# Kernel optimization log

Measured on AMD Instinct MI355X. Metric: run time of the kernel, lower is better.

The kernel has to match this reference:

```python
import jax, jax.numpy as jnp
import numpy as np

N = 131072   # number of points
C = 128      # channels
H = 8        # heads
D = C // H   # head dim = 16
K = 48       # patch (window) size
P = 3000     # number of path segments


def _build_indices():
    """Faithful numpy replica of PathAttention.get_padding_and_inverse (index-only, no_grad)."""
    rng = np.random.default_rng(0)
    lengths = rng.integers(K + 1, 3 * K, size=P)          # all > K -> padded to multiple of K
    M = int(lengths.sum())
    bpad = ((lengths + K - 1) // K) * K
    off = np.concatenate([[0], np.cumsum(lengths)])
    offp = np.concatenate([[0], np.cumsum(bpad)])
    Mpad = int(offp[-1])
    pad = np.arange(Mpad)
    unpad = np.arange(M)
    for i in range(P):
        o0, o1, p0, p1 = off[i], off[i + 1], offp[i], offp[i + 1]
        unpad[o0:o1] += p0 - o0
        b = int(lengths[i])
        if b != bpad[i]:
            r = b % K
            # replicate previous window's tail into the padded region
            pad[p1 - K + r:p1] = pad[p1 - 2 * K + r:p1 - K]
        pad[p0:p1] -= p0 - o0
    # every point appears at least once so the scatter-mean covers all N rows
    inv = np.concatenate([rng.permutation(N), rng.integers(0, N, M - N)])
    rng.shuffle(inv)
    return pad, unpad, inv


def setup_inputs() -> dict:
    pad, unpad, inv = _build_indices()
    M = unpad.shape[0]
    key = jax.random.key(0)
    ks = jax.random.split(key, 8)
    s = 0.02
    theta = jax.random.uniform(ks[1], (M, D), minval=0.0, maxval=2.0 * np.pi)
    return {
        "feat": jax.random.normal(ks[0], (N, C), jnp.float32),
        "cos": jnp.cos(theta).astype(jnp.float32),
        "sin": jnp.sin(theta).astype(jnp.float32),
        "g1": jnp.ones((C,), jnp.float32),
        "b1": jnp.zeros((C,), jnp.float32),
        "qkv_w": (jax.random.normal(ks[2], (3 * C, C)) * s).astype(jnp.float32),
        "qkv_b": jnp.zeros((3 * C,), jnp.float32),
        "proj_w": (jax.random.normal(ks[3], (C, C)) * s).astype(jnp.float32),
        "proj_b": jnp.zeros((C,), jnp.float32),
        "g2": jnp.ones((C,), jnp.float32),
        "b2": jnp.zeros((C,), jnp.float32),
        "fc1_w": (jax.random.normal(ks[4], (4 * C, C)) * s).astype(jnp.float32),
        "fc1_b": jnp.zeros((4 * C,), jnp.float32),
        "fc2_w": (jax.random.normal(ks[5], (C, 4 * C)) * s).astype(jnp.float32),
        "fc2_b": jnp.zeros((C,), jnp.float32),
        "path_inverse": jnp.asarray(inv, jnp.int32),
        "pad": jnp.asarray(pad, jnp.int32),
        "unpad": jnp.asarray(unpad, jnp.int32),
        "num_heads": H,
        "patch_size": K,
    }


def _ln(x, g, b):
    m = x.mean(-1, keepdims=True)
    v = x.var(-1, keepdims=True)
    return (x - m) / jnp.sqrt(v + 1e-5) * g + b


def reference(feat, cos, sin, g1, b1, qkv_w, qkv_b, proj_w, proj_b, g2, b2,
              fc1_w, fc1_b, fc2_w, fc2_b, path_inverse, pad, unpad,
              num_heads, patch_size):
    Np, Cc = feat.shape
    Hh = num_heads
    Dd = Cc // Hh
    Kk = patch_size
    # pre-norm + qkv projection, then path gather and pad gather
    h = _ln(feat, g1, b1)
    qkv = (h @ qkv_w.T + qkv_b)[path_inverse][pad]          # [Mpad, 3C]
    Mpad = qkv.shape[0]
    qkv = qkv.reshape(Mpad, 3, Hh, Dd)
    q, k, v = qkv[:, 0], qkv[:, 1], qkv[:, 2]               # [Mpad, H, D]
    # non-interleaved rope (flash-attn apply_rotary_emb with cos of dim D//2)
    cp = cos[pad][:, :Dd // 2][:, None, :]                  # [Mpad, 1, D/2]
    sp = sin[pad][:, :Dd // 2][:, None, :]
    def rope(x):
        x1, x2 = x[..., :Dd // 2], x[..., Dd // 2:]
        return jnp.concatenate([x1 * cp - x2 * sp, x2 * cp + x1 * sp], axis=-1)
    q = rope(q)
    k = rope(k)
    # windowed attention: all windows are exactly K after padding
    Wn = Mpad // Kk
    qw = q.reshape(Wn, Kk, Hh, Dd)
    kw = k.reshape(Wn, Kk, Hh, Dd)
    vw = v.reshape(Wn, Kk, Hh, Dd)
    scores = jnp.einsum('wqhd,wkhd->whqk', qw, kw) * (Dd ** -0.5)
    p = jax.nn.softmax(scores, axis=-1)
    o = jnp.einsum('whqk,wkhd->wqhd', p, vw).reshape(Mpad, Cc)
    # unpad gather, output projection, scatter-mean combine over overlapping paths
    o = o[unpad] @ proj_w.T + proj_b                        # [M, C]
    sums = jax.ops.segment_sum(o, path_inverse, num_segments=Np)
    cnt = jax.ops.segment_sum(jnp.ones((o.shape[0],), o.dtype), path_inverse, num_segments=Np)
    a = sums / jnp.maximum(cnt, 1.0)[:, None]
    x = feat + a
    # MLP branch
    h2 = _ln(x, g2, b2)
    m = jax.nn.gelu(h2 @ fc1_w.T + fc1_b, approximate=False) @ fc2_w.T + fc2_b
    return x + m
```

## Files before the change

### kernel.cpp

```cpp
#include <hip/hip_runtime.h>


typedef __attribute__((ext_vector_type(4))) float f32x4;
typedef __attribute__((ext_vector_type(8))) short bf16x8;
typedef __attribute__((ext_vector_type(4))) short bf16x4;

#define MFMA(a, b, c) __builtin_amdgcn_mfma_f32_16x16x32_bf16(a, b, c, 0, 0, 0)

static __device__ __forceinline__ short f2bf(float x) {
  union { float f; unsigned u; } v; v.f = x;
  unsigned r = v.u + 0x7FFFu + ((v.u >> 16) & 1u);
  return (short)(r >> 16);
}
static __device__ __forceinline__ float bf2f(short b) {
  union { unsigned u; float f; } v;
  v.u = ((unsigned)(unsigned short)b) << 16;
  return v.f;
}

__global__ void k_cvt(const float* __restrict__ s, short* __restrict__ d, int n) {
  int i = blockIdx.x * 256 + threadIdx.x;
  if (i < n) d[i] = f2bf(s[i]);
}

__global__ void k_cnt(const int* __restrict__ pinv, int* __restrict__ cnt, int M) {
  int i = blockIdx.x * 256 + threadIdx.x;
  if (i < M) atomicAdd(&cnt[pinv[i]], 1);
}

__global__ __launch_bounds__(256) void k_scan1(const int* __restrict__ cnt,
                                               int* __restrict__ lpre,
                                               int* __restrict__ bsum) {
  const int i = blockIdx.x * 256 + threadIdx.x;
  const int t = threadIdx.x, lane = t & 63, wid = t >> 6;
  int v = cnt[i];
  int x = v;
#pragma unroll
  for (int d = 1; d < 64; d <<= 1) {
    int y = __shfl_up(x, d);
    if (lane >= d) x += y;
  }
  __shared__ int wsum[4];
  if (lane == 63) wsum[wid] = x;
  __syncthreads();
  int add = 0;
#pragma unroll
  for (int wv = 0; wv < 4; wv++) add += (wv < wid) ? wsum[wv] : 0;
  lpre[i] = x + add - v;
  if (t == 255) bsum[blockIdx.x] = x + add;
}

__global__ __launch_bounds__(512) void k_scan2(int* __restrict__ bsum, int nb) {
  const int t = threadIdx.x, lane = t & 63, wid = t >> 6;
  int v = (t < nb) ? bsum[t] : 0;
  int x = v;
#pragma unroll
  for (int d = 1; d < 64; d <<= 1) {
    int y = __shfl_up(x, d);
    if (lane >= d) x += y;
  }
  __shared__ int wsum[8];
  if (lane == 63) wsum[wid] = x;
  __syncthreads();
  int add = 0;
#pragma unroll
  for (int wv = 0; wv < 8; wv++) add += (wv < wid) ? wsum[wv] : 0;
  if (t < nb) bsum[t] = x + add - v;
}

__global__ void k_place(const int* __restrict__ pinv, const int* __restrict__ lpre,
                        const int* __restrict__ bsum, int* __restrict__ cursor,
                        int* __restrict__ idxl, int M) {
  int m = blockIdx.x * 256 + threadIdx.x;
  if (m < M) {
    int n = pinv[m];
    int slot = atomicAdd(&cursor[n], 1);
    idxl[lpre[n] + bsum[n >> 8] + slot] = m;
  }
}

__global__ __launch_bounds__(256) void k1_ln_qkv(
    const float* __restrict__ feat, const float* __restrict__ g1,
    const float* __restrict__ b1, const short* __restrict__ wq,
    const float* __restrict__ bq, short* __restrict__ qkvb) {
  __shared__ short h_lds[32 * 128];
  __shared__ short o_st[32 * 384];
  const int blk = blockIdx.x, t = threadIdx.x;
  {
    const int r = t >> 3, oct = t & 7;
    const float* fp = feat + (size_t)(blk * 32 + r) * 128 + oct * 16;
    float vals[16];
    float s = 0.f, s2 = 0.f;
#pragma unroll
    for (int i = 0; i < 4; i++) {
      f32x4 v = *(const f32x4*)(fp + i * 4);
#pragma unroll
      for (int j = 0; j < 4; j++) { float x = v[j]; vals[i * 4 + j] = x; s += x; s2 += x * x; }
    }
    s += __shfl_xor(s, 1);  s += __shfl_xor(s, 2);  s += __shfl_xor(s, 4);
    s2 += __shfl_xor(s2, 1); s2 += __shfl_xor(s2, 2); s2 += __shfl_xor(s2, 4);
    float mean = s * (1.f / 128.f);
    float rstd = rsqrtf(s2 * (1.f / 128.f) - mean * mean + 1e-5f);
    const int sw = (r & 7) << 4;
#pragma unroll
    for (int gi = 0; gi < 2; gi++) {
      bf16x8 wv;
#pragma unroll
      for (int j = 0; j < 8; j++) {
        int c = oct * 16 + gi * 8 + j;
        wv[j] = f2bf((vals[gi * 8 + j] - mean) * rstd * g1[c] + b1[c]);
      }
      *(bf16x8*)((char*)h_lds + r * 256 + ((oct * 32 + gi * 16) ^ sw)) = wv;
    }
  }
  __syncthreads();
  const int wave = t >> 6, lane = t & 63, u = lane & 15, g = lane >> 4;
  f32x4 acc[2][6];
  f32x4 zz = {0.f, 0.f, 0.f, 0.f};
#pragma unroll
  for (int a = 0; a < 2; a++)
#pragma unroll
    for (int b = 0; b < 6; b++) acc[a][b] = zz;
#pragma unroll
  for (int kk = 0; kk < 4; kk++) {
    bf16x8 af[2];
#pragma unroll
    for (int rt = 0; rt < 2; rt++)
      af[rt] = *(const bf16x8*)((char*)h_lds + (rt * 16 + u) * 256 +
                                ((kk * 64 + g * 16) ^ ((u & 7) << 4)));
    bf16x8 bfr[6];
#pragma unroll
    for (int ct = 0; ct < 6; ct++) {
      int col = wave * 96 + ct * 16 + u;
      bfr[ct] = *(const bf16x8*)(wq + (size_t)col * 128 + kk * 32 + g * 8);
    }
#pragma unroll
    for (int rt = 0; rt < 2; rt++)
#pragma unroll
      for (int ct = 0; ct < 6; ct++) acc[rt][ct] = MFMA(af[rt], bfr[ct], acc[rt][ct]);
  }
#pragma unroll
  for (int rt = 0; rt < 2; rt++)
#pragma unroll
    for (int ct = 0; ct < 6; ct++) {
      int col = wave * 96 + ct * 16 + u;
      float bias = bq[col];
#pragma unroll
      for (int reg = 0; reg < 4; reg++) {
        int rowl = rt * 16 + 4 * g + reg;
        *(short*)((char*)o_st + rowl * 768 + ((col * 2) ^ (g << 5))) =
            f2bf(acc[rt][ct][reg] + bias);
      }
    }
  __syncthreads();
  for (int idx = t; idx < 1536; idx += 256) {
    int r = idx / 48, c8 = idx % 48;
    bf16x8 v = *(const bf16x8*)((char*)o_st + r * 768 +
                                ((c8 * 16) ^ ((((r >> 2) & 3)) << 5)));
    *(bf16x8*)(qkvb + ((size_t)blk * 32 + r) * 384 + c8 * 8) = v;
  }
}

__global__ __launch_bounds__(512) void k2_attn(
    const short* __restrict__ qkv, const float* __restrict__ cosb,
    const float* __restrict__ sinb, const int* __restrict__ pinv,
    const int* __restrict__ padv, const int* __restrict__ unpadv,
    short* __restrict__ ocmp) {
  __shared__ short qo_lds[48 * 136];
  __shared__ short k_lds[48 * 128];
  __shared__ short vT[8 * 16 * 64];
  __shared__ int midx_s[48];
  __shared__ int gidx_s[48];
  __shared__ int canon_s[48];
  __shared__ float cs_s[48 * 8];
  __shared__ float sn_s[48 * 8];

  const int w = blockIdx.x;
  const int t = threadIdx.x;

  if (t < 48) {
    int pp = w * 48 + t;
    int m = padv[pp];
    midx_s[t] = m;
    gidx_s[t] = pinv[m];
    canon_s[t] = (unpadv[m] == pp) ? 1 : 0;
    const float* cp = cosb + (size_t)m * 16;
    const float* sp = sinb + (size_t)m * 16;
#pragma unroll
    for (int i = 0; i < 2; i++) {
      *(f32x4*)(cs_s + t * 8 + i * 4) = *(const f32x4*)(cp + i * 4);
      *(f32x4*)(sn_s + t * 8 + i * 4) = *(const f32x4*)(sp + i * 4);
    }
  }
  __syncthreads();

  {
    const int r = t >> 3, seg = t & 7;
    if (r < 48) {
      const short* rowp = qkv + (size_t)gidx_s[r] * 384;
#pragma unroll
      for (int ci = 0; ci < 3; ci++) {
        const int c0 = seg * 48 + ci * 16;
        const int sec = c0 >> 7;
        const int hh = (c0 & 127) >> 4;
        bf16x8 lo = *(const bf16x8*)(rowp + c0);
        bf16x8 hi = *(const bf16x8*)(rowp + c0 + 8);
        if (sec < 2) {
          bf16x8 w0, w1;
#pragma unroll
          for (int j = 0; j < 8; j++) {
            float x1 = bf2f(lo[j]), x2 = bf2f(hi[j]);
            float cp = cs_s[r * 8 + j], sp2 = sn_s[r * 8 + j];
            w0[j] = f2bf(x1 * cp - x2 * sp2);
            w1[j] = f2bf(x2 * cp + x1 * sp2);
          }
          char* dst = (char*)(sec == 0 ? qo_lds : k_lds);
          int sw = (r & 7) << 4;
          *(bf16x8*)(dst + r * 256 + ((hh * 32) ^ sw)) = w0;
          *(bf16x8*)(dst + r * 256 + ((hh * 32 + 16) ^ sw)) = w1;
        } else {
#pragma unroll
          for (int d = 0; d < 16; d++) {
            short val = (d < 8) ? lo[d] : hi[d - 8];
            *(short*)((char*)vT + hh * 2048 + d * 128 + ((r * 2) ^ ((d & 7) << 3))) = val;
          }
        }
      }
    } else {
#pragma unroll
      for (int ci = 0; ci < 3; ci++) {
        const int c0 = seg * 48 + ci * 16;
        if (c0 >= 256) {
          const int hh = (c0 & 127) >> 4;
#pragma unroll
          for (int d = 0; d < 16; d++)
            *(short*)((char*)vT + hh * 2048 + d * 128 + ((r * 2) ^ ((d & 7) << 3))) = 0;
        }
      }
    }
  }
  __syncthreads();

  const int h = t >> 6, lane = t & 63, u = lane & 15, g = lane >> 4;
  const int sbase = h * 32 + g * 16;
  bf16x8 zf = {0, 0, 0, 0, 0, 0, 0, 0};
  bf16x8 kf[3], qf[3];
#pragma unroll
  for (int i = 0; i < 3; i++) {
    int kj = i * 16 + u;
    if (g < 2) {
      kf[i] = *(const bf16x8*)((char*)k_lds + kj * 256 + (sbase ^ ((kj & 7) << 4)));
      qf[i] = *(const bf16x8*)((char*)qo_lds + kj * 256 + (sbase ^ ((kj & 7) << 4)));
    } else { kf[i] = zf; qf[i] = zf; }
  }
  union UU { bf16x8 v8; bf16x4 v4[2]; };
  UU a1, a2;
  {
    const int dbase = h * 2048 + u * 128;
    const int sw = (u & 7) << 3;
    a1.v4[0] = *(const bf16x4*)((char*)vT + dbase + ((8 * g) ^ sw));
    a1.v4[1] = *(const bf16x4*)((char*)vT + dbase + ((32 + 8 * g) ^ sw));
    a2.v4[0] = *(const bf16x4*)((char*)vT + dbase + ((64 + 8 * g) ^ sw));
    a2.v4[1] = *(const bf16x4*)((char*)vT + dbase + ((96 + 8 * g) ^ sw));
  }
  __syncthreads();

  f32x4 d1[3][3];
#pragma unroll
  for (int a = 0; a < 3; a++)
#pragma unroll
    for (int b = 0; b < 3; b++) {
      f32x4 z = {0.f, 0.f, 0.f, 0.f};
      d1[a][b] = MFMA(kf[a], qf[b], z);
    }

  float rl[3];
#pragma unroll
  for (int qt = 0; qt < 3; qt++) {
    float mx = -3.0e38f;
#pragma unroll
    for (int kt = 0; kt < 3; kt++)
#pragma unroll
      for (int rr = 0; rr < 4; rr++) {
        float sv = d1[kt][qt][rr] * 0.25f;
        d1[kt][qt][rr] = sv;
        mx = fmaxf(mx, sv);
      }
    mx = fmaxf(mx, __shfl_xor(mx, 16));
    mx = fmaxf(mx, __shfl_xor(mx, 32));
    float sm = 0.f;
#pragma unroll
    for (int kt = 0; kt < 3; kt++)
#pragma unroll
      for (int rr = 0; rr < 4; rr++) {
        float e = __expf(d1[kt][qt][rr] - mx);
        d1[kt][qt][rr] = e;
        sm += e;
      }
    sm += __shfl_xor(sm, 16);
    sm += __shfl_xor(sm, 32);
    rl[qt] = 1.0f / sm;
  }

#pragma unroll
  for (int qt = 0; qt < 3; qt++) {
    UU bu1, bu2;
#pragma unroll
    for (int i = 0; i < 4; i++) {
      bu1.v8[i] = f2bf(d1[0][qt][i]);
      bu1.v8[i + 4] = f2bf(d1[1][qt][i]);
      bu2.v8[i] = f2bf(d1[2][qt][i]);
      bu2.v8[i + 4] = 0;
    }
    f32x4 z = {0.f, 0.f, 0.f, 0.f};
    f32x4 acc = MFMA(a1.v8, bu1.v8, z);
    acc = MFMA(a2.v8, bu2.v8, acc);
#pragma unroll
    for (int reg = 0; reg < 4; reg++)
      *(short*)((char*)qo_lds + (qt * 16 + u) * 272 + h * 32 + g * 8 + reg * 2) =
          f2bf(acc[reg] * rl[qt]);
  }
  __syncthreads();
  for (int idx = t; idx < 768; idx += 512) {
    int r = idx >> 4, c8 = idx & 15;
    if (canon_s[r]) {
      *(bf16x8*)(ocmp + (size_t)midx_s[r] * 128 + c8 * 8) =
          *(const bf16x8*)((char*)qo_lds + r * 272 + c8 * 16);
    }
  }
}

__global__ __launch_bounds__(256) void k3_proj(
    const short* __restrict__ ocmp, const short* __restrict__ wp,
    const float* __restrict__ pb, short* __restrict__ oproj, int M) {
  __shared__ short o_st[64 * 128];
  const int blk = blockIdx.x, t = threadIdx.x;
  const int m0 = blk * 64;
  const int wave = t >> 6, lane = t & 63, u = lane & 15, g = lane >> 4;
  f32x4 acc[4][2];
  f32x4 zz = {0.f, 0.f, 0.f, 0.f};
#pragma unroll
  for (int a = 0; a < 4; a++) { acc[a][0] = zz; acc[a][1] = zz; }
  bf16x8 zf = {0, 0, 0, 0, 0, 0, 0, 0};
#pragma unroll
  for (int kk = 0; kk < 4; kk++) {
    bf16x8 af[4];
#pragma unroll
    for (int rt = 0; rt < 4; rt++) {
      int m = m0 + rt * 16 + u;
      af[rt] = (m < M) ? *(const bf16x8*)(ocmp + (size_t)m * 128 + kk * 32 + g * 8) : zf;
    }
    bf16x8 bfr[2];
#pragma unroll
    for (int ct = 0; ct < 2; ct++) {
      int col = wave * 32 + ct * 16 + u;
      bfr[ct] = *(const bf16x8*)(wp + (size_t)col * 128 + kk * 32 + g * 8);
    }
#pragma unroll
    for (int rt = 0; rt < 4; rt++)
#pragma unroll
      for (int ct = 0; ct < 2; ct++) acc[rt][ct] = MFMA(af[rt], bfr[ct], acc[rt][ct]);
  }
#pragma unroll
  for (int rt = 0; rt < 4; rt++)
#pragma unroll
    for (int ct = 0; ct < 2; ct++) {
      int col = wave * 32 + ct * 16 + u;
      float bias = pb[col];
#pragma unroll
      for (int reg = 0; reg < 4; reg++) {
        int rowl = rt * 16 + 4 * g + reg;
        *(short*)((char*)o_st + rowl * 256 + ((col * 2) ^ (g << 5))) =
            f2bf(acc[rt][ct][reg] + bias);
      }
    }
  __syncthreads();
#pragma unroll
  for (int it = 0; it < 4; it++) {
    int idx = t + it * 256;
    int r = idx >> 4, c8 = idx & 15;
    if (m0 + r < M) {
      bf16x8 v = *(const bf16x8*)((char*)o_st + r * 256 +
                                  ((c8 * 16) ^ (((r >> 2) & 3) << 5)));
      *(bf16x8*)(oproj + (size_t)(m0 + r) * 128 + c8 * 8) = v;
    }
  }
}

__global__ __launch_bounds__(256) void k4_fused(
    const float* __restrict__ feat, float* __restrict__ dout,
    const int* __restrict__ cnt, const int* __restrict__ lpre,
    const int* __restrict__ bsum, const int* __restrict__ idxl,
    const short* __restrict__ oproj,
    const float* __restrict__ g2, const float* __restrict__ b2,
    const short* __restrict__ w1, const float* __restrict__ bb1,
    const short* __restrict__ w2, const float* __restrict__ bb2) {
  __shared__ short m_lds[32 * 512];
  const int blk = blockIdx.x, t = threadIdx.x;
  const int wave = t >> 6, lane = t & 63, u = lane & 15, g = lane >> 4;

  {
    const int r = t >> 3, oct = t & 7;
    const int n = blk * 32 + r;
    const int c = cnt[n];
    const int start = lpre[n] + bsum[n >> 8];
    float sum[16];
#pragma unroll
    for (int i = 0; i < 16; i++) sum[i] = 0.f;
    for (int j = 0; j < c; j++) {
      int m = idxl[start + j];
      const short* op = oproj + (size_t)m * 128 + oct * 16;
      bf16x8 v0 = *(const bf16x8*)op;
      bf16x8 v1 = *(const bf16x8*)(op + 8);
#pragma unroll
      for (int q = 0; q < 8; q++) { sum[q] += bf2f(v0[q]); sum[8 + q] += bf2f(v1[q]); }
    }
    const float rc = 1.0f / fmaxf((float)c, 1.0f);
    const float* fp = feat + (size_t)n * 128 + oct * 16;
    float* xp = dout + (size_t)n * 128 + oct * 16;
    float vals[16];
    float s = 0.f, s2 = 0.f;
#pragma unroll
    for (int i = 0; i < 4; i++) {
      f32x4 fv = *(const f32x4*)(fp + i * 4);
      f32x4 xv;
#pragma unroll
      for (int j = 0; j < 4; j++) {
        float x = fv[j] + sum[i * 4 + j] * rc;
        xv[j] = x; vals[i * 4 + j] = x; s += x; s2 += x * x;
      }
      *(f32x4*)(xp + i * 4) = xv;
    }
    s += __shfl_xor(s, 1);  s += __shfl_xor(s, 2);  s += __shfl_xor(s, 4);
    s2 += __shfl_xor(s2, 1); s2 += __shfl_xor(s2, 2); s2 += __shfl_xor(s2, 4);
    float mean = s * (1.f / 128.f);
    float rstd = rsqrtf(s2 * (1.f / 128.f) - mean * mean + 1e-5f);
    const int sw = (r & 7) << 4;
#pragma unroll
    for (int gi = 0; gi < 2; gi++) {
      bf16x8 wv;
#pragma unroll
      for (int j = 0; j < 8; j++) {
        int cc = oct * 16 + gi * 8 + j;
        wv[j] = f2bf((vals[gi * 8 + j] - mean) * rstd * g2[cc] + b2[cc]);
      }
      *(bf16x8*)((char*)m_lds + r * 256 + ((oct * 32 + gi * 16) ^ sw)) = wv;
    }
  }
  __syncthreads();

  f32x4 acc[2][8];
  f32x4 zz = {0.f, 0.f, 0.f, 0.f};
#pragma unroll
  for (int a = 0; a < 2; a++)
#pragma unroll
    for (int b = 0; b < 8; b++) acc[a][b] = zz;
#pragma unroll
  for (int kk = 0; kk < 4; kk++) {
    bf16x8 af[2];
#pragma unroll
    for (int rt = 0; rt < 2; rt++)
      af[rt] = *(const bf16x8*)((char*)m_lds + (rt * 16 + u) * 256 +
                                ((kk * 64 + g * 16) ^ ((u & 7) << 4)));
    bf16x8 bfr[8];
#pragma unroll
    for (int ct = 0; ct < 8; ct++) {
      int col = wave * 128 + ct * 16 + u;
      bfr[ct] = *(const bf16x8*)(w1 + (size_t)col * 128 + kk * 32 + g * 8);
    }
#pragma unroll
    for (int rt = 0; rt < 2; rt++)
#pragma unroll
      for (int ct = 0; ct < 8; ct++) acc[rt][ct] = MFMA(af[rt], bfr[ct], acc[rt][ct]);
  }
  __syncthreads();

#pragma unroll
  for (int rt = 0; rt < 2; rt++)
#pragma unroll
    for (int ct = 0; ct < 8; ct++) {
      int col = wave * 128 + ct * 16 + u;
      float bias = bb1[col];
#pragma unroll
      for (int reg = 0; reg < 4; reg++) {
        int rowl = rt * 16 + 4 * g + reg;
        float v = acc[rt][ct][reg] + bias;
        v = 0.5f * v * (1.0f + erff(v * 0.70710678118654752f));
        *(short*)((char*)m_lds + rowl * 1024 + ((col * 2) ^ ((rowl & 7) << 4))) = f2bf(v);
      }
    }
  __syncthreads();

  f32x4 acc2[2][2];
#pragma unroll
  for (int a = 0; a < 2; a++) { acc2[a][0] = zz; acc2[a][1] = zz; }
#pragma unroll
  for (int kk = 0; kk < 16; kk++) {
    bf16x8 af2[2];
#pragma unroll
    for (int rt = 0; rt < 2; rt++)
      af2[rt] = *(const bf16x8*)((char*)m_lds + (rt * 16 + u) * 1024 +
                                 ((kk * 64 + g * 16) ^ ((u & 7) << 4)));
#pragma unroll
    for (int ct = 0; ct < 2; ct++) {
      int col = wave * 32 + ct * 16 + u;
      bf16x8 bfr = *(const bf16x8*)(w2 + (size_t)col * 512 + kk * 32 + g * 8);
#pragma unroll
      for (int rt = 0; rt < 2; rt++) acc2[rt][ct] = MFMA(af2[rt], bfr, acc2[rt][ct]);
    }
  }
#pragma unroll
  for (int rt = 0; rt < 2; rt++)
#pragma unroll
    for (int ct = 0; ct < 2; ct++) {
      int col = wave * 32 + ct * 16 + u;
      float bias = bb2[col];
#pragma unroll
      for (int reg = 0; reg < 4; reg++) {
        size_t rr = (size_t)blk * 32 + rt * 16 + 4 * g + reg;
        float* p = dout + rr * 128 + col;
        *p = *p + acc2[rt][ct][reg] + bias;
      }
    }
}

extern "C" void kernel_launch(void* const* d_in, const int* in_sizes, int n_in,
                              void* d_out, int out_size, void* d_ws, size_t ws_size,
                              hipStream_t stream) {
  (void)n_in; (void)out_size; (void)ws_size;
  const float* feat   = (const float*)d_in[0];
  const float* cosb   = (const float*)d_in[1];
  const float* sinb   = (const float*)d_in[2];
  const float* g1     = (const float*)d_in[3];
  const float* b1     = (const float*)d_in[4];
  const float* qkv_w  = (const float*)d_in[5];
  const float* qkv_b  = (const float*)d_in[6];
  const float* proj_w = (const float*)d_in[7];
  const float* proj_b = (const float*)d_in[8];
  const float* g2     = (const float*)d_in[9];
  const float* b2     = (const float*)d_in[10];
  const float* fc1_w  = (const float*)d_in[11];
  const float* fc1_b  = (const float*)d_in[12];
  const float* fc2_w  = (const float*)d_in[13];
  const float* fc2_b  = (const float*)d_in[14];
  const int* pinv     = (const int*)d_in[15];
  const int* padv     = (const int*)d_in[16];
  const int* unpadv   = (const int*)d_in[17];

  const int N    = in_sizes[0] / 128;
  const int M    = in_sizes[15];
  const int Mpad = in_sizes[16];
  const int Wn   = Mpad / 48;

  float* dout = (float*)d_out;
  char* ws = (char*)d_ws;

  size_t szQ = (size_t)N * 384 * 2;
  size_t szO = (size_t)M * 128 * 2;

  short* qkvb  = (short*)ws;
  short* oproj = (short*)ws;
  short* ocmp  = (short*)(ws + szQ);

  size_t offI = ((size_t)M * 256 + 255) & ~(size_t)255;
  int* cnt    = (int*)(ws + offI);
  int* cursor = cnt + N;
  int* lpre   = cursor + N;
  int* bsum   = lpre + N;
  int* idxl   = bsum + 1024;

  size_t offW = szQ + szO;
  short* wq_b = (short*)(ws + offW);
  short* wp_b = wq_b + 49152;
  short* w1_b = wp_b + 16384;
  short* w2_b = w1_b + 65536;

  k_cvt<<<(49152 + 255) / 256, 256, 0, stream>>>(qkv_w, wq_b, 49152);
  k_cvt<<<(16384 + 255) / 256, 256, 0, stream>>>(proj_w, wp_b, 16384);
  k_cvt<<<(65536 + 255) / 256, 256, 0, stream>>>(fc1_w, w1_b, 65536);
  k_cvt<<<(65536 + 255) / 256, 256, 0, stream>>>(fc2_w, w2_b, 65536);

  k1_ln_qkv<<<N / 32, 256, 0, stream>>>(feat, g1, b1, wq_b, qkv_b, qkvb);
  k2_attn<<<Wn, 512, 0, stream>>>(qkvb, cosb, sinb, pinv, padv, unpadv, ocmp);

  hipMemsetAsync(cnt, 0, (size_t)N * 4, stream);
  hipMemsetAsync(cursor, 0, (size_t)N * 4, stream);
  k_cnt<<<(M + 255) / 256, 256, 0, stream>>>(pinv, cnt, M);
  k_scan1<<<N / 256, 256, 0, stream>>>(cnt, lpre, bsum);
  k_scan2<<<1, 512, 0, stream>>>(bsum, N / 256);
  k_place<<<(M + 255) / 256, 256, 0, stream>>>(pinv, lpre, bsum, cursor, idxl, M);

  k3_proj<<<(M + 63) / 64, 256, 0, stream>>>(ocmp, wp_b, proj_b, oproj, M);
  k4_fused<<<N / 32, 256, 0, stream>>>(feat, dout, cnt, lpre, bsum, idxl, oproj,
                                       g2, b2, w1_b, fc1_b, w2_b, fc2_b);
}
```

Measured before the change: 480.6 us.

## Split gather+LN2 from MLP into separate kernels via global bf16 buffer

Splits the fused scatter-mean/LN2/MLP kernel into a gather+layernorm kernel that writes normalized bf16 rows to a workspace buffer, and an MLP kernel that reads its A operands directly from that buffer. The aim is to let the latency-bound irregular gather run without the large LDS allocation limiting occupancy, and to decouple it from the MFMA-heavy MLP. In exchange it adds an extra global write and read of the hidden activations and one more launch.

Result: slower. 493.1 us (+2.6%).

```diff
diff --git a/kernel.cpp b/kernel.cpp
--- a/kernel.cpp
+++ b/kernel.cpp
@@ -387,68 +387,69 @@
   }
 }
 
-__global__ __launch_bounds__(256) void k4_fused(
+__global__ __launch_bounds__(256) void k4a_gather_ln(
     const float* __restrict__ feat, float* __restrict__ dout,
     const int* __restrict__ cnt, const int* __restrict__ lpre,
     const int* __restrict__ bsum, const int* __restrict__ idxl,
     const short* __restrict__ oproj,
     const float* __restrict__ g2, const float* __restrict__ b2,
-    const short* __restrict__ w1, const float* __restrict__ bb1,
-    const short* __restrict__ w2, const float* __restrict__ bb2) {
+    short* __restrict__ hbuf) {
+  const int t = threadIdx.x;
+  const int r = t >> 3, oct = t & 7;
+  const int n = blockIdx.x * 32 + r;
+  const int c = cnt[n];
+  const int start = lpre[n] + bsum[n >> 8];
+  float sum[16];
+#pragma unroll
+  for (int i = 0; i < 16; i++) sum[i] = 0.f;
+  for (int j = 0; j < c; j++) {
+    int m = idxl[start + j];
+    const short* op = oproj + (size_t)m * 128 + oct * 16;
+    bf16x8 v0 = *(const bf16x8*)op;
+    bf16x8 v1 = *(const bf16x8*)(op + 8);
+#pragma unroll
+    for (int q = 0; q < 8; q++) { sum[q] += bf2f(v0[q]); sum[8 + q] += bf2f(v1[q]); }
+  }
+  const float rc = 1.0f / fmaxf((float)c, 1.0f);
+  const float* fp = feat + (size_t)n * 128 + oct * 16;
+  float* xp = dout + (size_t)n * 128 + oct * 16;
+  float vals[16];
+  float s = 0.f, s2 = 0.f;
+#pragma unroll
+  for (int i = 0; i < 4; i++) {
+    f32x4 fv = *(const f32x4*)(fp + i * 4);
+    f32x4 xv;
+#pragma unroll
+    for (int j = 0; j < 4; j++) {
+      float x = fv[j] + sum[i * 4 + j] * rc;
+      xv[j] = x; vals[i * 4 + j] = x; s += x; s2 += x * x;
+    }
+    *(f32x4*)(xp + i * 4) = xv;
+  }
+  s += __shfl_xor(s, 1);  s += __shfl_xor(s, 2);  s += __shfl_xor(s, 4);
+  s2 += __shfl_xor(s2, 1); s2 += __shfl_xor(s2, 2); s2 += __shfl_xor(s2, 4);
+  float mean = s * (1.f / 128.f);
+  float rstd = rsqrtf(s2 * (1.f / 128.f) - mean * mean + 1e-5f);
+  bf16x8 h0, h1;
+#pragma unroll
+  for (int j = 0; j < 8; j++) {
+    int c0 = oct * 16 + j, c1 = oct * 16 + 8 + j;
+    h0[j] = f2bf((vals[j] - mean) * rstd * g2[c0] + b2[c0]);
+    h1[j] = f2bf((vals[8 + j] - mean) * rstd * g2[c1] + b2[c1]);
+  }
+  short* hp = hbuf + (size_t)n * 128 + oct * 16;
+  *(bf16x8*)hp = h0;
+  *(bf16x8*)(hp + 8) = h1;
+}
+
+__global__ __launch_bounds__(256) void k4b_mlp(
+    const short* __restrict__ hbuf, const short* __restrict__ w1,
+    const float* __restrict__ bb1, const short* __restrict__ w2,
+    const float* __restrict__ bb2, float* __restrict__ dout) {
   __shared__ short m_lds[32 * 512];
   const int blk = blockIdx.x, t = threadIdx.x;
   const int wave = t >> 6, lane = t & 63, u = lane & 15, g = lane >> 4;
 
-  {
-    const int r = t >> 3, oct = t & 7;
-    const int n = blk * 32 + r;
-    const int c = cnt[n];
-    const int start = lpre[n] + bsum[n >> 8];
-    float sum[16];
-#pragma unroll
-    for (int i = 0; i < 16; i++) sum[i] = 0.f;
-    for (int j = 0; j < c; j++) {
-      int m = idxl[start + j];
-      const short* op = oproj + (size_t)m * 128 + oct * 16;
-      bf16x8 v0 = *(const bf16x8*)op;
-      bf16x8 v1 = *(const bf16x8*)(op + 8);
-#pragma unroll
-      for (int q = 0; q < 8; q++) { sum[q] += bf2f(v0[q]); sum[8 + q] += bf2f(v1[q]); }
-    }
-    const float rc = 1.0f / fmaxf((float)c, 1.0f);
-    const float* fp = feat + (size_t)n * 128 + oct * 16;
-    float* xp = dout + (size_t)n * 128 + oct * 16;
-    float vals[16];
-    float s = 0.f, s2 = 0.f;
-#pragma unroll
-    for (int i = 0; i < 4; i++) {
-      f32x4 fv = *(const f32x4*)(fp + i * 4);
-      f32x4 xv;
-#pragma unroll
-      for (int j = 0; j < 4; j++) {
-        float x = fv[j] + sum[i * 4 + j] * rc;
-        xv[j] = x; vals[i * 4 + j] = x; s += x; s2 += x * x;
-      }
-      *(f32x4*)(xp + i * 4) = xv;
-    }
-    s += __shfl_xor(s, 1);  s += __shfl_xor(s, 2);  s += __shfl_xor(s, 4);
-    s2 += __shfl_xor(s2, 1); s2 += __shfl_xor(s2, 2); s2 += __shfl_xor(s2, 4);
-    float mean = s * (1.f / 128.f);
-    float rstd = rsqrtf(s2 * (1.f / 128.f) - mean * mean + 1e-5f);
-    const int sw = (r & 7) << 4;
-#pragma unroll
-    for (int gi = 0; gi < 2; gi++) {
-      bf16x8 wv;
-#pragma unroll
-      for (int j = 0; j < 8; j++) {
-        int cc = oct * 16 + gi * 8 + j;
-        wv[j] = f2bf((vals[gi * 8 + j] - mean) * rstd * g2[cc] + b2[cc]);
-      }
-      *(bf16x8*)((char*)m_lds + r * 256 + ((oct * 32 + gi * 16) ^ sw)) = wv;
-    }
-  }
-  __syncthreads();
-
   f32x4 acc[2][8];
   f32x4 zz = {0.f, 0.f, 0.f, 0.f};
 #pragma unroll
@@ -460,8 +461,8 @@
     bf16x8 af[2];
 #pragma unroll
     for (int rt = 0; rt < 2; rt++)
-      af[rt] = *(const bf16x8*)((char*)m_lds + (rt * 16 + u) * 256 +
-                                ((kk * 64 + g * 16) ^ ((u & 7) << 4)));
+      af[rt] = *(const bf16x8*)(hbuf + (size_t)(blk * 32 + rt * 16 + u) * 128 +
+                                kk * 32 + g * 8);
     bf16x8 bfr[8];
 #pragma unroll
     for (int ct = 0; ct < 8; ct++) {
@@ -473,7 +474,6 @@
 #pragma unroll
       for (int ct = 0; ct < 8; ct++) acc[rt][ct] = MFMA(af[rt], bfr[ct], acc[rt][ct]);
   }
-  __syncthreads();
 
 #pragma unroll
   for (int rt = 0; rt < 2; rt++)
@@ -561,6 +561,7 @@
   short* qkvb  = (short*)ws;
   short* oproj = (short*)ws;
   short* ocmp  = (short*)(ws + szQ);
+  short* hbuf  = (short*)(ws + szQ);
 
   size_t offI = ((size_t)M * 256 + 255) & ~(size_t)255;
   int* cnt    = (int*)(ws + offI);
@@ -591,6 +592,7 @@
   k_place<<<(M + 255) / 256, 256, 0, stream>>>(pinv, lpre, bsum, cursor, idxl, M);
 
   k3_proj<<<(M + 63) / 64, 256, 0, stream>>>(ocmp, wp_b, proj_b, oproj, M);
-  k4_fused<<<N / 32, 256, 0, stream>>>(feat, dout, cnt, lpre, bsum, idxl, oproj,
-                                       g2, b2, w1_b, fc1_b, w2_b, fc2_b);
-}
+  k4a_gather_ln<<<N / 32, 256, 0, stream>>>(feat, dout, cnt, lpre, bsum, idxl,
+                                            oproj, g2, b2, hbuf);
+  k4b_mlp<<<N / 32, 256, 0, stream>>>(hbuf, w1_b, fc1_b, w2_b, fc2_b, dout);
+}
```
